# Performance work log

Measured on AMD Instinct MI355X. Metric: run time of the kernel, lower is better.

## Reference

```python
import jax, jax.numpy as jnp
import numpy as np

B, D, N, C = 256, 2048, 65536, 8192  # batch, feat dim, memory-bank size, num clusters
TEMP = 0.05


def setup_inputs() -> dict:
    key = jax.random.key(0)
    k1, k2, k3, k4 = jax.random.split(key, 4)
    inputs = jax.random.normal(k1, (B, D), jnp.float32)
    inputs = inputs / jnp.linalg.norm(inputs, axis=1, keepdims=True)
    features = jax.random.normal(k2, (N, D), jnp.float32)
    features = features / jnp.linalg.norm(features, axis=1, keepdims=True)
    labels = jax.random.randint(k3, (N,), 0, C).astype(jnp.int64)
    labels = labels.at[0].set(C - 1)  # pin labels.max()+1 == C (torch uses data-dependent size)
    indexes = jax.random.randint(k4, (B,), 0, N).astype(jnp.int64)
    return {"inputs": inputs, "indexes": indexes, "features": features, "labels": labels}


def reference(inputs, indexes, features, labels):
    # HM.forward: similarity of batch against full memory bank (momentum update is a
    # backward-pass buffer side effect, not part of the differentiable graph)
    sims = inputs @ features.T                                   # [B, N]
    targets = labels[indexes]                                    # [B]
    # per-sample soft cluster centers over same-label memory entries
    attn_mask = (targets[:, None] == labels[None, :]).astype(sims.dtype)  # [B, N]
    centers = (attn_mask * sims) @ features                      # [B, D]
    diag = jnp.einsum('bd,bd->b', inputs, centers) / TEMP        # diag of inputs_raw @ centers.T / temp
    logits = sims / TEMP                                         # [B, N]
    # cluster-averaged similarities: index_add over labels == segment_sum
    sim = jax.ops.segment_sum(logits.T, labels, num_segments=C)  # [C, B]
    nums = jax.ops.segment_sum(jnp.ones((N,), logits.dtype), labels, num_segments=C)  # [C]
    cmask = (nums > 0).astype(logits.dtype)                      # [C]
    sim = sim / jnp.where(nums > 0, nums, 1.0)[:, None]
    # replace each sample's own-cluster entry with its center similarity
    cols = jnp.arange(B)
    onehot = jnp.zeros((C, B), logits.dtype).at[targets, cols].set(1.0)
    score = jnp.zeros((C, B), logits.dtype).at[targets, cols].set(diag)
    sim = sim * (1.0 - onehot) + score                           # [C, B]
    # masked softmax over clusters (unstabilized exp, faithful to original)
    exps = jnp.exp(sim.T) * cmask[None, :]                       # [B, C]
    masked_sim = exps / (exps.sum(axis=1, keepdims=True) + 1e-6)
    logp = jnp.log(masked_sim + 1e-6)
    return -jnp.mean(logp[cols, targets])                        # nll_loss, mean reduction
```

## Files before the change

kernel.cpp:

```cpp
#include <hip/hip_runtime.h>

#define BATCH 256
#define DIM   2048
#define NMEM  65536
#define NCLUS 8192
#define TEMP  0.05f

typedef __attribute__((ext_vector_type(8))) short bf16x8;
typedef __attribute__((ext_vector_type(4))) float f32x4;
typedef __attribute__((ext_vector_type(4))) unsigned short u16x4;
typedef __attribute__((ext_vector_type(8))) unsigned short u16x8;

__device__ inline unsigned short f2bf(float f) {
    unsigned u = __float_as_uint(f);
    u += 0x7fffu + ((u >> 16) & 1u);
    return (unsigned short)(u >> 16);
}
__device__ inline float bf2f(unsigned short u) {
    return __uint_as_float(((unsigned)u) << 16);
}

__global__ void k_init(const int* __restrict__ labels, const int* __restrict__ indexes,
                       int* __restrict__ nums, int* __restrict__ targets) {
    int gid = blockIdx.x * 256 + threadIdx.x;
    if (gid < NMEM) atomicAdd(&nums[labels[gid]], 1);
    if (gid < BATCH) targets[gid] = labels[indexes[gid]];
}

__global__ void k_scan(const int* __restrict__ nums, int* __restrict__ offs) {
    __shared__ int part[256];
    int t = threadIdx.x;
    int base = t * 32;
    int local[32];
    int s = 0;
    #pragma unroll
    for (int i = 0; i < 32; i++) { local[i] = s; s += nums[base + i]; }
    part[t] = s;
    __syncthreads();
    for (int d = 1; d < 256; d <<= 1) {
        int v = (t >= d) ? part[t - d] : 0;
        __syncthreads();
        part[t] += v;
        __syncthreads();
    }
    int cb = (t == 0) ? 0 : part[t - 1];
    #pragma unroll
    for (int i = 0; i < 32; i++) offs[base + i] = cb + local[i];
}

__global__ void k_scatter(const int* __restrict__ labels, const int* __restrict__ offs,
                          int* __restrict__ cursor, int* __restrict__ order) {
    int n = blockIdx.x * 256 + threadIdx.x;
    int c = labels[n];
    int pos = atomicAdd(&cursor[c], 1);
    order[offs[c] + pos] = n;
}

__global__ void k_convA(const float* __restrict__ inputs, unsigned short* __restrict__ A_sw) {
    int gid = blockIdx.x * 256 + threadIdx.x;
    int e = gid * 8;
    int r = e >> 11;
    int k = e & 2047;
    const float4* p = (const float4*)(inputs + (size_t)r * DIM + k);
    float4 f0 = p[0], f1 = p[1];
    u16x8 o;
    o[0] = f2bf(f0.x); o[1] = f2bf(f0.y); o[2] = f2bf(f0.z); o[3] = f2bf(f0.w);
    o[4] = f2bf(f1.x); o[5] = f2bf(f1.y); o[6] = f2bf(f1.z); o[7] = f2bf(f1.w);
    *(u16x8*)(A_sw + (size_t)(k >> 5) * (BATCH * 32) + r * 32 + (k & 31)) = o;
}

__global__ __launch_bounds__(256) void k_gemm(const float* __restrict__ feats,
                                              const unsigned short* __restrict__ A_sw,
                                              unsigned short* __restrict__ sims_t) {
    __shared__ short As[BATCH * 32];
    __shared__ short Bs[64 * 32];
    int tid = threadIdx.x;
    int w = tid >> 6, l = tid & 63;
    int n0 = blockIdx.x * 64;
    int ar = l & 15, aq = l >> 4;

    f32x4 acc[4][4];
    #pragma unroll
    for (int i = 0; i < 4; i++)
        #pragma unroll
        for (int j = 0; j < 4; j++) acc[i][j] = (f32x4){0.f, 0.f, 0.f, 0.f};

    const float* fb = feats + (size_t)(n0 + (tid >> 3)) * DIM + (tid & 7) * 4;
    int brow = tid >> 3, bcol = (tid & 7) * 4;

    for (int s = 0; s < 64; s++) {
        __syncthreads();
        {
            const char* gbase = (const char*)A_sw + (size_t)s * 16384;
            #pragma unroll
            for (int i = 0; i < 4; i++) {
                int ofs = ((w << 2) + i) * 1024;
                __builtin_amdgcn_global_load_lds(
                    (const __attribute__((address_space(1))) void*)(gbase + ofs + l * 16),
                    (__attribute__((address_space(3))) void*)((char*)As + ofs),
                    16, 0, 0);
            }
        }
        {
            float4 v0 = *(const float4*)(fb + s * 32);
            float4 v1 = *(const float4*)(fb + (size_t)32 * DIM + s * 32);
            u16x4 b0, b1;
            b0[0] = f2bf(v0.x); b0[1] = f2bf(v0.y); b0[2] = f2bf(v0.z); b0[3] = f2bf(v0.w);
            b1[0] = f2bf(v1.x); b1[1] = f2bf(v1.y); b1[2] = f2bf(v1.z); b1[3] = f2bf(v1.w);
            *(u16x4*)&Bs[brow * 32 + bcol] = b0;
            *(u16x4*)&Bs[(brow + 32) * 32 + bcol] = b1;
        }
        __syncthreads();
        bf16x8 a[4], b[4];
        #pragma unroll
        for (int i = 0; i < 4; i++) a[i] = *(const bf16x8*)&As[(w * 64 + i * 16 + ar) * 32 + aq * 8];
        #pragma unroll
        for (int j = 0; j < 4; j++) b[j] = *(const bf16x8*)&Bs[(j * 16 + ar) * 32 + aq * 8];
        #pragma unroll
        for (int i = 0; i < 4; i++)
            #pragma unroll
            for (int j = 0; j < 4; j++)
                acc[i][j] = __builtin_amdgcn_mfma_f32_16x16x32_bf16(a[i], b[j], acc[i][j], 0, 0, 0);
    }
    #pragma unroll
    for (int i = 0; i < 4; i++) {
        int row = w * 64 + i * 16 + aq * 4;
        #pragma unroll
        for (int j = 0; j < 4; j++) {
            int col = n0 + j * 16 + ar;
            f32x4 v = acc[i][j];
            u16x4 o;
            o[0] = f2bf(v[0]); o[1] = f2bf(v[1]); o[2] = f2bf(v[2]); o[3] = f2bf(v[3]);
            *(u16x4*)&sims_t[(size_t)col * BATCH + row] = o;
        }
    }
}

__global__ void k_reduce(const unsigned short* __restrict__ sims_t, const int* __restrict__ order,
                         const int* __restrict__ offs, const int* __restrict__ nums,
                         const int* __restrict__ targets, float* __restrict__ partial,
                         float* __restrict__ numval) {
    int c = blockIdx.x;
    int cnt = nums[c];
    if (cnt == 0) return;
    int t = threadIdx.x;
    int off = offs[c];
    bool own = (targets[t] == c);
    float acc = 0.f, d2 = 0.f;
    for (int i = 0; i < cnt; i++) {
        int n = order[off + i];
        float s = bf2f(sims_t[(size_t)n * BATCH + t]);
        acc += s;
        if (own) d2 += s * s;
    }
    float val = own ? __expf(d2 * (1.f / TEMP)) : __expf(acc / ((float)cnt * TEMP));
    if (own) numval[t] = val;
    atomicAdd(&partial[(c & 63) * BATCH + t], val);
}

__global__ void k_loss(const float* __restrict__ partial, const float* __restrict__ numval,
                       float* __restrict__ out) {
    __shared__ float red[256];
    int t = threadIdx.x;
    float tot = 0.f;
    #pragma unroll
    for (int p = 0; p < 64; p++) tot += partial[p * BATCH + t];
    float ls = -logf(numval[t] / (tot + 1e-6f) + 1e-6f);
    red[t] = ls;
    __syncthreads();
    for (int d = 128; d > 0; d >>= 1) {
        if (t < d) red[t] += red[t + d];
        __syncthreads();
    }
    if (t == 0) out[0] = red[0] / (float)BATCH;
}

extern "C" void kernel_launch(void* const* d_in, const int* in_sizes, int n_in,
                              void* d_out, int out_size, void* d_ws, size_t ws_size,
                              hipStream_t stream) {
    const float* inputs  = (const float*)d_in[0];
    const int*   indexes = (const int*)d_in[1];
    const float* feats   = (const float*)d_in[2];
    const int*   labels  = (const int*)d_in[3];
    float* out = (float*)d_out;

    char* ws = (char*)d_ws;
    size_t off = 0;
    unsigned short* sims_t = (unsigned short*)(ws + off); off += (size_t)NMEM * BATCH * 2;
    unsigned short* A_sw   = (unsigned short*)(ws + off); off += (size_t)BATCH * DIM * 2;
    int*   nums    = (int*)(ws + off);   off += NCLUS * 4;
    int*   cursor  = (int*)(ws + off);   off += NCLUS * 4;
    float* partial = (float*)(ws + off); off += 64 * BATCH * 4;
    int*   offs    = (int*)(ws + off);   off += NCLUS * 4;
    int*   order   = (int*)(ws + off);   off += (size_t)NMEM * 4;
    int*   targets = (int*)(ws + off);   off += BATCH * 4;
    float* numval  = (float*)(ws + off); off += BATCH * 4;

    hipMemsetAsync(nums, 0, NCLUS * 4 + NCLUS * 4 + 64 * BATCH * 4, stream);

    k_init   <<<NMEM / 256, 256, 0, stream>>>(labels, indexes, nums, targets);
    k_scan   <<<1, 256, 0, stream>>>(nums, offs);
    k_scatter<<<NMEM / 256, 256, 0, stream>>>(labels, offs, cursor, order);
    k_convA  <<<(BATCH * DIM / 8) / 256, 256, 0, stream>>>(inputs, A_sw);
    k_gemm   <<<NMEM / 64, 256, 0, stream>>>(feats, A_sw, sims_t);
    k_reduce <<<NCLUS, 256, 0, stream>>>(sims_t, order, offs, nums, targets, partial, numval);
    k_loss   <<<1, 256, 0, stream>>>(partial, numval, out);
}
```

Measured before the change: 810.3 us.

## Aggregate features per cluster before GEMM, shrinking GEMM from N to C columns

Uses linearity to sum the memory-bank features within each cluster first (k_agg), then runs a split-K bf16 GEMM of inputs against the 8192 cluster sums instead of all 65536 features. The own-cluster diagonal term is computed separately in k_diag with exact fp32 dot products over that cluster's members. This removes the large B×N bf16 sims write/read and cuts GEMM FLOPs by about 8x. In exchange it adds a full streaming pass over the features and fp32 split-K partial outputs, and it rounds the cluster sums to bf16.

Measured after the change: 807.6 us. About the same (-0.3%).

```diff
diff --git a/kernel.cpp b/kernel.cpp
--- a/kernel.cpp
+++ b/kernel.cpp
@@ -15,9 +15,6 @@
     unsigned u = __float_as_uint(f);
     u += 0x7fffu + ((u >> 16) & 1u);
     return (unsigned short)(u >> 16);
-}
-__device__ inline float bf2f(unsigned short u) {
-    return __uint_as_float(((unsigned)u) << 16);
 }
 
 __global__ void k_init(const int* __restrict__ labels, const int* __restrict__ indexes,
@@ -69,14 +66,39 @@
     *(u16x8*)(A_sw + (size_t)(k >> 5) * (BATCH * 32) + r * 32 + (k & 31)) = o;
 }
 
-__global__ __launch_bounds__(256) void k_gemm(const float* __restrict__ feats,
-                                              const unsigned short* __restrict__ A_sw,
-                                              unsigned short* __restrict__ sims_t) {
+__global__ __launch_bounds__(256) void k_agg(const float* __restrict__ feats,
+                                             const int* __restrict__ order,
+                                             const int* __restrict__ offs,
+                                             const int* __restrict__ nums,
+                                             unsigned short* __restrict__ csum) {
+    int c = blockIdx.x;
+    int t = threadIdx.x;
+    int cnt = nums[c], off = offs[c];
+    float acc[8] = {0.f, 0.f, 0.f, 0.f, 0.f, 0.f, 0.f, 0.f};
+    int nn = (cnt > 0) ? order[off] : 0;
+    for (int i = 0; i < cnt; i++) {
+        int ncur = nn;
+        if (i + 1 < cnt) nn = order[off + i + 1];
+        const float4* p = (const float4*)(feats + (size_t)ncur * DIM + t * 8);
+        float4 a = p[0], b = p[1];
+        acc[0] += a.x; acc[1] += a.y; acc[2] += a.z; acc[3] += a.w;
+        acc[4] += b.x; acc[5] += b.y; acc[6] += b.z; acc[7] += b.w;
+    }
+    u16x8 o;
+    #pragma unroll
+    for (int j = 0; j < 8; j++) o[j] = f2bf(acc[j]);
+    *(u16x8*)(csum + (size_t)c * DIM + t * 8) = o;
+}
+
+__global__ __launch_bounds__(256) void k_gemm2(const unsigned short* __restrict__ csum,
+                                               const unsigned short* __restrict__ A_sw,
+                                               float* __restrict__ simP) {
     __shared__ short As[BATCH * 32];
     __shared__ short Bs[64 * 32];
     int tid = threadIdx.x;
     int w = tid >> 6, l = tid & 63;
     int n0 = blockIdx.x * 64;
+    int kc = blockIdx.y;
     int ar = l & 15, aq = l >> 4;
 
     f32x4 acc[4][4];
@@ -85,10 +107,10 @@
         #pragma unroll
         for (int j = 0; j < 4; j++) acc[i][j] = (f32x4){0.f, 0.f, 0.f, 0.f};
 
-    const float* fb = feats + (size_t)(n0 + (tid >> 3)) * DIM + (tid & 7) * 4;
-    int brow = tid >> 3, bcol = (tid & 7) * 4;
-
-    for (int s = 0; s < 64; s++) {
+    const char* bgbase = (const char*)(csum + (size_t)(n0 + (tid >> 2)) * DIM + (tid & 3) * 8);
+
+    for (int ss = 0; ss < 16; ss++) {
+        int s = kc * 16 + ss;
         __syncthreads();
         {
             const char* gbase = (const char*)A_sw + (size_t)s * 16384;
@@ -102,13 +124,10 @@
             }
         }
         {
-            float4 v0 = *(const float4*)(fb + s * 32);
-            float4 v1 = *(const float4*)(fb + (size_t)32 * DIM + s * 32);
-            u16x4 b0, b1;
-            b0[0] = f2bf(v0.x); b0[1] = f2bf(v0.y); b0[2] = f2bf(v0.z); b0[3] = f2bf(v0.w);
-            b1[0] = f2bf(v1.x); b1[1] = f2bf(v1.y); b1[2] = f2bf(v1.z); b1[3] = f2bf(v1.w);
-            *(u16x4*)&Bs[brow * 32 + bcol] = b0;
-            *(u16x4*)&Bs[(brow + 32) * 32 + bcol] = b1;
+            __builtin_amdgcn_global_load_lds(
+                (const __attribute__((address_space(1))) void*)(bgbase + (size_t)s * 64),
+                (__attribute__((address_space(3))) void*)((char*)Bs + w * 1024),
+                16, 0, 0);
         }
         __syncthreads();
         bf16x8 a[4], b[4];
@@ -122,40 +141,65 @@
             for (int j = 0; j < 4; j++)
                 acc[i][j] = __builtin_amdgcn_mfma_f32_16x16x32_bf16(a[i], b[j], acc[i][j], 0, 0, 0);
     }
+    float* outp = simP + (size_t)kc * (NCLUS * BATCH);
     #pragma unroll
     for (int i = 0; i < 4; i++) {
         int row = w * 64 + i * 16 + aq * 4;
         #pragma unroll
         for (int j = 0; j < 4; j++) {
             int col = n0 + j * 16 + ar;
-            f32x4 v = acc[i][j];
-            u16x4 o;
-            o[0] = f2bf(v[0]); o[1] = f2bf(v[1]); o[2] = f2bf(v[2]); o[3] = f2bf(v[3]);
-            *(u16x4*)&sims_t[(size_t)col * BATCH + row] = o;
-        }
-    }
-}
-
-__global__ void k_reduce(const unsigned short* __restrict__ sims_t, const int* __restrict__ order,
-                         const int* __restrict__ offs, const int* __restrict__ nums,
-                         const int* __restrict__ targets, float* __restrict__ partial,
-                         float* __restrict__ numval) {
-    int c = blockIdx.x;
-    int cnt = nums[c];
-    if (cnt == 0) return;
-    int t = threadIdx.x;
-    int off = offs[c];
-    bool own = (targets[t] == c);
-    float acc = 0.f, d2 = 0.f;
+            *(f32x4*)&outp[(size_t)col * BATCH + row] = acc[i][j];
+        }
+    }
+}
+
+__global__ void k_diag(const float* __restrict__ inputs, const float* __restrict__ feats,
+                       const int* __restrict__ order, const int* __restrict__ offs,
+                       const int* __restrict__ nums, const int* __restrict__ targets,
+                       float* __restrict__ numval) {
+    int b = blockIdx.x, t = threadIdx.x;
+    int c = targets[b];
+    int cnt = nums[c], off = offs[c];
+    const float4* ip = (const float4*)(inputs + (size_t)b * DIM + t * 8);
+    float4 x0 = ip[0], x1 = ip[1];
+    __shared__ float red[256];
+    float d2 = 0.f;
     for (int i = 0; i < cnt; i++) {
         int n = order[off + i];
-        float s = bf2f(sims_t[(size_t)n * BATCH + t]);
-        acc += s;
-        if (own) d2 += s * s;
-    }
-    float val = own ? __expf(d2 * (1.f / TEMP)) : __expf(acc / ((float)cnt * TEMP));
-    if (own) numval[t] = val;
-    atomicAdd(&partial[(c & 63) * BATCH + t], val);
+        const float4* fp = (const float4*)(feats + (size_t)n * DIM + t * 8);
+        float4 a = fp[0], bb = fp[1];
+        float part = x0.x * a.x + x0.y * a.y + x0.z * a.z + x0.w * a.w
+                   + x1.x * bb.x + x1.y * bb.y + x1.z * bb.z + x1.w * bb.w;
+        red[t] = part;
+        __syncthreads();
+        for (int d = 128; d > 0; d >>= 1) {
+            if (t < d) red[t] += red[t + d];
+            __syncthreads();
+        }
+        if (t == 0) { float dot = red[0]; d2 += dot * dot; }
+        __syncthreads();
+    }
+    if (t == 0) numval[b] = __expf(d2 * (1.f / TEMP));
+}
+
+__global__ void k_reduce2(const float* __restrict__ simP, const int* __restrict__ nums,
+                          const int* __restrict__ targets, const float* __restrict__ numval,
+                          float* __restrict__ partial) {
+    int p = blockIdx.x, t = threadIdx.x;
+    int tgt = targets[t];
+    float nv = numval[t];
+    float tot = 0.f;
+    const size_t CB = (size_t)NCLUS * BATCH;
+    for (int j = 0; j < 128; j++) {
+        int c = p * 128 + j;
+        int cnt = nums[c];
+        if (cnt == 0) continue;
+        size_t a = (size_t)c * BATCH + t;
+        float s = simP[a] + simP[CB + a] + simP[2 * CB + a] + simP[3 * CB + a];
+        float val = (tgt == c) ? nv : __expf(s / ((float)cnt * TEMP));
+        tot += val;
+    }
+    partial[p * 256 + t] = tot;
 }
 
 __global__ void k_loss(const float* __restrict__ partial, const float* __restrict__ numval,
@@ -164,7 +208,7 @@
     int t = threadIdx.x;
     float tot = 0.f;
     #pragma unroll
-    for (int p = 0; p < 64; p++) tot += partial[p * BATCH + t];
+    for (int p = 0; p < 64; p++) tot += partial[p * 256 + t];
     float ls = -logf(numval[t] / (tot + 1e-6f) + 1e-6f);
     red[t] = ls;
     __syncthreads();
@@ -186,23 +230,27 @@
 
     char* ws = (char*)d_ws;
     size_t off = 0;
-    unsigned short* sims_t = (unsigned short*)(ws + off); off += (size_t)NMEM * BATCH * 2;
-    unsigned short* A_sw   = (unsigned short*)(ws + off); off += (size_t)BATCH * DIM * 2;
+    unsigned short* csum = (unsigned short*)(ws + off); off += (size_t)NCLUS * DIM * 2;
+    unsigned short* A_sw = (unsigned short*)(ws + off); off += (size_t)BATCH * DIM * 2;
+    float* simP    = (float*)(ws + off); off += (size_t)4 * NCLUS * BATCH * 4;
     int*   nums    = (int*)(ws + off);   off += NCLUS * 4;
     int*   cursor  = (int*)(ws + off);   off += NCLUS * 4;
-    float* partial = (float*)(ws + off); off += 64 * BATCH * 4;
     int*   offs    = (int*)(ws + off);   off += NCLUS * 4;
     int*   order   = (int*)(ws + off);   off += (size_t)NMEM * 4;
     int*   targets = (int*)(ws + off);   off += BATCH * 4;
+    float* partial = (float*)(ws + off); off += 64 * BATCH * 4;
     float* numval  = (float*)(ws + off); off += BATCH * 4;
 
-    hipMemsetAsync(nums, 0, NCLUS * 4 + NCLUS * 4 + 64 * BATCH * 4, stream);
+    hipMemsetAsync(nums, 0, NCLUS * 4 + NCLUS * 4, stream);
 
     k_init   <<<NMEM / 256, 256, 0, stream>>>(labels, indexes, nums, targets);
     k_scan   <<<1, 256, 0, stream>>>(nums, offs);
     k_scatter<<<NMEM / 256, 256, 0, stream>>>(labels, offs, cursor, order);
     k_convA  <<<(BATCH * DIM / 8) / 256, 256, 0, stream>>>(inputs, A_sw);
-    k_gemm   <<<NMEM / 64, 256, 0, stream>>>(feats, A_sw, sims_t);
-    k_reduce <<<NCLUS, 256, 0, stream>>>(sims_t, order, offs, nums, targets, partial, numval);
+    k_agg    <<<NCLUS, 256, 0, stream>>>(feats, order, offs, nums, csum);
+    dim3 g2(NCLUS / 64, 4);
+    k_gemm2  <<<g2, 256, 0, stream>>>(csum, A_sw, simP);
+    k_diag   <<<BATCH, 256, 0, stream>>>(inputs, feats, order, offs, nums, targets, numval);
+    k_reduce2<<<64, 256, 0, stream>>>(simP, nums, targets, numval, partial);
     k_loss   <<<1, 256, 0, stream>>>(partial, numval, out);
 }
```
